# Optimization experiments

Hardware: AMD Instinct MI355X
Metric: run time of the kernel (lower is better)

The kernel has to match this reference:

```python
import jax, jax.numpy as jnp
import numpy as np


def setup_inputs() -> dict:
    key = jax.random.key(0)
    k1, k2 = jax.random.split(key)
    B, N, M = 4, 16384, 4096
    src_points = jax.random.normal(k1, (B, N, 3), dtype=jnp.float32)
    target_verts = jax.random.normal(k2, (B, M, 3), dtype=jnp.float32)
    return {"src_points": src_points, "target_verts": target_verts}


def reference(src_points, target_verts):
    # target_faces=None path of ChamferLoss: degenerate one-vertex triangles,
    # so closest-point-on-mesh == nearest target vertex.
    # d2[b,n,m] = ||p_bn - v_bm||^2 via the expansion p2 + v2 - 2 p.v
    p2 = jnp.sum(src_points * src_points, axis=-1)          # (B, N)
    v2 = jnp.sum(target_verts * target_verts, axis=-1)      # (B, M)
    pv = jnp.einsum('bnd,bmd->bnm', src_points, target_verts)  # (B, N, M)
    d2 = p2[:, :, None] + v2[:, None, :] - 2.0 * pv
    d2 = jnp.maximum(d2, 0.0)
    min_d2 = jnp.min(d2, axis=-1)                            # (B, N)
    num_src_per_batch = src_points.shape[1]
    loss = jnp.sum(min_d2, axis=-1) / num_src_per_batch      # (B,)
    return loss
```

## Files before the change

kernel.cpp:

```cpp
#include <hip/hip_runtime.h>
#include <float.h>


typedef __bf16 bf16x8 __attribute__((ext_vector_type(8)));
typedef float  f32x16 __attribute__((ext_vector_type(16)));

constexpr int B = 4, N = 16384, M = 4096;
constexpr int BN = B * N;
constexpr int NCHUNK = 16;
constexpr int CHUNK_V = M / NCHUNK;
constexpr int TILES = CHUNK_V / 32;
constexpr int TPB = 256;
constexpr int Q = 4;
constexpr int PPW = 32 * Q;
constexpr int PPB = 4 * PPW;
constexpr int PBLK = BN / PPB;

__device__ __forceinline__ void write_vert(char* bp, int u,
                                           float x, float y, float z) {
    __bf16 xh = (__bf16)x, yh = (__bf16)y, zh = (__bf16)z;
    float xhf = (float)xh, yhf = (float)yh, zhf = (float)zh;
    __bf16 xl = (__bf16)(x - xhf), yl = (__bf16)(y - yhf), zl = (__bf16)(z - zhf);
    float v2 = fmaf(x, x, fmaf(y, y, z * z));
    __bf16 v2h = (__bf16)v2;
    __bf16 v2l = (__bf16)(v2 - (float)v2h);
    __bf16 zero = (__bf16)0.0f;
    bf16x8 h0, h1;
    h0[0] = (__bf16)(-2.0f * xhf); h0[1] = (__bf16)(-2.0f * yhf);
    h0[2] = (__bf16)(-2.0f * zhf);
    h0[3] = h0[0]; h0[4] = h0[1]; h0[5] = h0[2];
    h0[6] = (__bf16)(-2.0f * (float)xl); h0[7] = (__bf16)(-2.0f * (float)yl);
    h1[0] = (__bf16)(-2.0f * (float)zl); h1[1] = v2h; h1[2] = v2l;
    h1[3] = zero; h1[4] = zero; h1[5] = zero; h1[6] = zero; h1[7] = zero;
    char* base = bp + ((u >> 5) << 10) + ((u & 31) << 4);
    *(bf16x8*)base         = h0;
    *(bf16x8*)(base + 512) = h1;
}

__global__ __launch_bounds__(TPB) void chamfer_mfma(
    const float* __restrict__ src, const float* __restrict__ tv,
    float* __restrict__ partial, float* __restrict__ out)
{
    __shared__ char lds[TILES * 1024];
    const int blk   = blockIdx.x;
    const int chunk = blk & 15;
    const int pblk  = blk >> 4;
    const int b     = pblk >> 5;
    const int t     = threadIdx.x;
    const int w     = t >> 6, L = t & 63;
    const int half  = L >> 5, c = L & 31;

    if (blk == 0 && t < B) out[t] = 0.0f;

    {
        const float* vs = tv + ((size_t)b * M + (size_t)chunk * CHUNK_V) * 3 + 3 * t;
        write_vert(lds, t, vs[0], vs[1], vs[2]);
    }

    const int pbase = pblk * PPB + w * PPW;
    __bf16 one = (__bf16)1.0f, zero = (__bf16)0.0f;
    bf16x8 bP[Q];
    float pp[Q];
#pragma unroll
    for (int q = 0; q < Q; ++q) {
        const int gp = pbase + q * 32 + c;
        float x = src[3 * gp], y = src[3 * gp + 1], z = src[3 * gp + 2];
        pp[q] = fmaf(x, x, fmaf(y, y, z * z));
        __bf16 xh = (__bf16)x, yh = (__bf16)y, zh = (__bf16)z;
        __bf16 xl = (__bf16)(x - (float)xh), yl = (__bf16)(y - (float)yh),
               zl = (__bf16)(z - (float)zh);
        bf16x8 f;
        if (half == 0) { f[0]=xh; f[1]=yh; f[2]=zh; f[3]=xl; f[4]=yl; f[5]=zl; f[6]=xh; f[7]=yh; }
        else { f[0]=zh; f[1]=one; f[2]=one; f[3]=zero; f[4]=zero; f[5]=zero; f[6]=zero; f[7]=zero; }
        bP[q] = f;
    }

    float mn[Q][8];
#pragma unroll
    for (int q = 0; q < Q; ++q)
#pragma unroll
        for (int u = 0; u < 8; ++u) mn[q][u] = FLT_MAX;
    f32x16 zeroC;
#pragma unroll
    for (int r = 0; r < 16; ++r) zeroC[r] = 0.0f;

    __syncthreads();

    const int laneoff = half * 512 + c * 16;
#pragma unroll 2
    for (int tl = 0; tl < TILES; ++tl) {
        bf16x8 av = *(const bf16x8*)(lds + tl * 1024 + laneoff);
#pragma unroll
        for (int q = 0; q < Q; ++q) {
            f32x16 C = __builtin_amdgcn_mfma_f32_32x32x16_bf16(av, bP[q], zeroC, 0, 0, 0);
#pragma unroll
            for (int u = 0; u < 8; ++u)
                mn[q][u] = fminf(fminf(mn[q][u], C[2 * u]), C[2 * u + 1]);
        }
    }

    float m[Q];
#pragma unroll
    for (int q = 0; q < Q; ++q) {
        float a = fminf(fminf(mn[q][0], mn[q][1]), fminf(mn[q][2], mn[q][3]));
        float d = fminf(fminf(mn[q][4], mn[q][5]), fminf(mn[q][6], mn[q][7]));
        float x = fminf(a, d);
        m[q] = fminf(x, __shfl_xor(x, 32, 64)) + pp[q];
    }
    float* pout = partial + (size_t)chunk * BN + pbase;
    if (L < 32) {
        pout[c]      = m[0];
        pout[32 + c] = m[1];
    } else {
        pout[64 + c] = m[2];
        pout[96 + c] = m[3];
    }
}

__global__ __launch_bounds__(256) void chamfer_reduce(
    const float* __restrict__ partial, float* __restrict__ out)
{
    const int p = blockIdx.x * 256 + threadIdx.x;
    const int b = blockIdx.x >> 6;
    float m = FLT_MAX;
#pragma unroll
    for (int cgr = 0; cgr < NCHUNK; ++cgr)
        m = fminf(m, partial[(size_t)cgr * BN + p]);
    float sum = fmaxf(m, 0.0f);

    for (int off = 32; off > 0; off >>= 1)
        sum += __shfl_down(sum, off, 64);
    __shared__ float acc[4];
    if ((threadIdx.x & 63) == 0) acc[threadIdx.x >> 6] = sum;
    __syncthreads();
    if (threadIdx.x == 0) {
        float s = acc[0] + acc[1] + acc[2] + acc[3];
        atomicAdd(&out[b], s * (1.0f / N));
    }
}

extern "C" void kernel_launch(void* const* d_in, const int* in_sizes, int n_in,
                              void* d_out, int out_size, void* d_ws, size_t ws_size,
                              hipStream_t stream) {
    const float* src = (const float*)d_in[0];
    const float* tv  = (const float*)d_in[1];
    float* out = (float*)d_out;
    float* partial = (float*)d_ws;

    chamfer_mfma  <<<PBLK * NCHUNK, TPB, 0, stream>>>(src, tv, partial, out);
    chamfer_reduce<<<BN / 256, 256, 0, stream>>>(partial, out);
}
```

Measured before the change: 74.89 us.

## Precompute vertex bf16 fragments in a separate kernel and double points per wave

Adds a pre-pass kernel that converts target vertices into split-bf16 MFMA fragment layout in global workspace once, so each MFMA block just copies 8KB into LDS instead of recomputing the conversion per block. It also doubles Q from 4 to 8 point tiles per wave, halving the block count and increasing reuse of each loaded vertex fragment across more MFMAs. The costs are an extra kernel launch, more registers for the accumulators (mn grows to 64 floats), and possibly lower occupancy.

```diff
diff --git a/kernel.cpp b/kernel.cpp
--- a/kernel.cpp
+++ b/kernel.cpp
@@ -11,13 +11,20 @@
 constexpr int CHUNK_V = M / NCHUNK;
 constexpr int TILES = CHUNK_V / 32;
 constexpr int TPB = 256;
-constexpr int Q = 4;
+constexpr int Q = 8;
 constexpr int PPW = 32 * Q;
 constexpr int PPB = 4 * PPW;
 constexpr int PBLK = BN / PPB;
+constexpr size_t BFRAG_BYTES = (size_t)B * M * 32;
 
-__device__ __forceinline__ void write_vert(char* bp, int u,
-                                           float x, float y, float z) {
+__global__ __launch_bounds__(256) void chamfer_pre(
+    const float* __restrict__ tv, unsigned char* __restrict__ bfr,
+    float* __restrict__ out)
+{
+    if (blockIdx.x == 0 && threadIdx.x < B) out[threadIdx.x] = 0.0f;
+    int i = blockIdx.x * 256 + threadIdx.x;
+    int m = i & (M - 1);
+    float x = tv[3 * i + 0], y = tv[3 * i + 1], z = tv[3 * i + 2];
     __bf16 xh = (__bf16)x, yh = (__bf16)y, zh = (__bf16)z;
     float xhf = (float)xh, yhf = (float)yh, zhf = (float)zh;
     __bf16 xl = (__bf16)(x - xhf), yl = (__bf16)(y - yhf), zl = (__bf16)(z - zhf);
@@ -25,6 +32,7 @@
     __bf16 v2h = (__bf16)v2;
     __bf16 v2l = (__bf16)(v2 - (float)v2h);
     __bf16 zero = (__bf16)0.0f;
+
     bf16x8 h0, h1;
     h0[0] = (__bf16)(-2.0f * xhf); h0[1] = (__bf16)(-2.0f * yhf);
     h0[2] = (__bf16)(-2.0f * zhf);
@@ -32,30 +40,31 @@
     h0[6] = (__bf16)(-2.0f * (float)xl); h0[7] = (__bf16)(-2.0f * (float)yl);
     h1[0] = (__bf16)(-2.0f * (float)zl); h1[1] = v2h; h1[2] = v2l;
     h1[3] = zero; h1[4] = zero; h1[5] = zero; h1[6] = zero; h1[7] = zero;
-    char* base = bp + ((u >> 5) << 10) + ((u & 31) << 4);
-    *(bf16x8*)base         = h0;
-    *(bf16x8*)(base + 512) = h1;
+
+    int chunk = m >> 8, local = m & (CHUNK_V - 1), tile = local >> 5;
+    size_t base = (size_t)(i >> 12) * 131072 + (size_t)chunk * 8192
+                + tile * 1024 + (m & 31) * 16;
+    *(bf16x8*)(bfr + base)       = h0;
+    *(bf16x8*)(bfr + base + 512) = h1;
 }
 
 __global__ __launch_bounds__(TPB) void chamfer_mfma(
-    const float* __restrict__ src, const float* __restrict__ tv,
-    float* __restrict__ partial, float* __restrict__ out)
+    const float* __restrict__ src, const unsigned char* __restrict__ bfr,
+    float* __restrict__ partial)
 {
-    __shared__ char lds[TILES * 1024];
+    __shared__ uint4 lds4[512];
+    const char* ldsc = (const char*)lds4;
     const int blk   = blockIdx.x;
     const int chunk = blk & 15;
     const int pblk  = blk >> 4;
-    const int b     = pblk >> 5;
+    const int b     = pblk >> 4;
     const int t     = threadIdx.x;
     const int w     = t >> 6, L = t & 63;
     const int half  = L >> 5, c = L & 31;
 
-    if (blk == 0 && t < B) out[t] = 0.0f;
-
-    {
-        const float* vs = tv + ((size_t)b * M + (size_t)chunk * CHUNK_V) * 3 + 3 * t;
-        write_vert(lds, t, vs[0], vs[1], vs[2]);
-    }
+    const uint4* gsrc = (const uint4*)(bfr + (size_t)b * 131072 + (size_t)chunk * 8192);
+    lds4[t]       = gsrc[t];
+    lds4[256 + t] = gsrc[256 + t];
 
     const int pbase = pblk * PPB + w * PPW;
     __bf16 one = (__bf16)1.0f, zero = (__bf16)0.0f;
@@ -89,7 +98,7 @@
     const int laneoff = half * 512 + c * 16;
 #pragma unroll 2
     for (int tl = 0; tl < TILES; ++tl) {
-        bf16x8 av = *(const bf16x8*)(lds + tl * 1024 + laneoff);
+        bf16x8 av = *(const bf16x8*)(ldsc + tl * 1024 + laneoff);
 #pragma unroll
         for (int q = 0; q < Q; ++q) {
             f32x16 C = __builtin_amdgcn_mfma_f32_32x32x16_bf16(av, bP[q], zeroC, 0, 0, 0);
@@ -99,21 +108,14 @@
         }
     }
 
-    float m[Q];
+    float* pout = partial + (size_t)chunk * BN + pbase;
 #pragma unroll
     for (int q = 0; q < Q; ++q) {
         float a = fminf(fminf(mn[q][0], mn[q][1]), fminf(mn[q][2], mn[q][3]));
         float d = fminf(fminf(mn[q][4], mn[q][5]), fminf(mn[q][6], mn[q][7]));
         float x = fminf(a, d);
-        m[q] = fminf(x, __shfl_xor(x, 32, 64)) + pp[q];
-    }
-    float* pout = partial + (size_t)chunk * BN + pbase;
-    if (L < 32) {
-        pout[c]      = m[0];
-        pout[32 + c] = m[1];
-    } else {
-        pout[64 + c] = m[2];
-        pout[96 + c] = m[3];
+        float m = fminf(x, __shfl_xor(x, 32, 64)) + pp[q];
+        if (L < 32) pout[q * 32 + c] = m;
     }
 }
 
@@ -145,8 +147,10 @@
     const float* src = (const float*)d_in[0];
     const float* tv  = (const float*)d_in[1];
     float* out = (float*)d_out;
-    float* partial = (float*)d_ws;
+    unsigned char* bfr = (unsigned char*)d_ws;
+    float* partial = (float*)((char*)d_ws + BFRAG_BYTES);
 
-    chamfer_mfma  <<<PBLK * NCHUNK, TPB, 0, stream>>>(src, tv, partial, out);
+    chamfer_pre   <<<(B * M) / 256, 256, 0, stream>>>(tv, bfr, out);
+    chamfer_mfma  <<<PBLK * NCHUNK, TPB, 0, stream>>>(src, bfr, partial);
     chamfer_reduce<<<BN / 256, 256, 0, stream>>>(partial, out);
 }
```

Result: slower. 80.60 us (+7.6%).
